# Kernel tuning notes

Hardware: AMD Instinct MI355X
Metric: run time of the kernel (lower is better)

The kernel has to match this reference:

```python
import jax, jax.numpy as jnp
import numpy as np

N_NODES = 100000
N_EDGES = 3200000
N_GRAPHS = 512
IN_DIM = 29   # NUM_COMPONENT_TYPES(15) + NUM_PARAMS(14)
HID = 128
LAT = 256


def setup_inputs() -> dict:
    key = jax.random.key(0)
    ks = jax.random.split(key, 16)
    x = jax.random.normal(ks[0], (N_NODES, IN_DIM), dtype=jnp.float32)
    edge_index = jax.random.randint(ks[1], (2, N_EDGES), 0, N_NODES, dtype=jnp.int64)
    batch = jnp.sort(jax.random.randint(ks[2], (N_NODES,), 0, N_GRAPHS, dtype=jnp.int64))

    def lin(k, fan_in, fan_out):
        kw, kb = jax.random.split(k)
        s = 1.0 / np.sqrt(fan_in)
        W = jax.random.uniform(kw, (fan_in, fan_out), minval=-s, maxval=s, dtype=jnp.float32)
        b = jax.random.uniform(kb, (fan_out,), minval=-s, maxval=s, dtype=jnp.float32)
        return W, b

    W1, b1 = lin(ks[3], IN_DIM, HID)
    W2, b2 = lin(ks[4], HID, HID)
    W3, b3 = lin(ks[5], HID, HID)
    Wmu, bmu = lin(ks[6], HID, LAT)
    Wlv, blv = lin(ks[7], HID, LAT)
    return {"x": x, "edge_index": edge_index, "batch": batch,
            "W1": W1, "b1": b1, "W2": W2, "b2": b2, "W3": W3, "b3": b3,
            "Wmu": Wmu, "bmu": bmu, "Wlv": Wlv, "blv": blv}


def _gcn_conv(h, W, b, src, dst, dis):
    # PyG GCNConv: out = D^-1/2 (A + I) D^-1/2 (h W) + b
    hw = h @ W                                   # [N, out]
    norm = dis[src] * dis[dst]                   # [E]
    agg = jax.ops.segment_sum(hw[src] * norm[:, None], dst, num_segments=h.shape[0])
    return agg + hw * (dis * dis)[:, None] + b   # self-loop term has norm dis[i]^2


def reference(x, edge_index, batch, W1, b1, W2, b2, W3, b3, Wmu, bmu, Wlv, blv):
    src, dst = edge_index[0], edge_index[1]
    # symmetric degree with self-loops (computed once, identical across layers)
    deg = jax.ops.segment_sum(jnp.ones(src.shape[0], jnp.float32), dst,
                              num_segments=x.shape[0]) + 1.0
    dis = jax.lax.rsqrt(deg)

    h = jax.nn.relu(_gcn_conv(x, W1, b1, src, dst, dis))
    h = jax.nn.relu(_gcn_conv(h, W2, b2, src, dst, dis))
    h = jax.nn.relu(_gcn_conv(h, W3, b3, src, dst, dis))

    # global_mean_pool over graph ids
    sums = jax.ops.segment_sum(h, batch, num_segments=N_GRAPHS)
    cnts = jax.ops.segment_sum(jnp.ones(h.shape[0], jnp.float32), batch,
                               num_segments=N_GRAPHS)
    pooled = sums / jnp.maximum(cnts, 1.0)[:, None]   # [G, HID]

    mu = pooled @ Wmu + bmu
    logvar = pooled @ Wlv + blv
    return (mu, logvar)
```

## Files before the change

### kernel.cpp

```cpp
#include <hip/hip_runtime.h>
#include <hip/hip_bf16.h>

#define N_NODES 100000
#define N_EDGES 3200000
#define N_GRAPHS 512
#define IN_DIM 29
#define HID 128
#define LAT 256
#define NB 391
#define CAP 9216

typedef unsigned int uint;
typedef unsigned short ushort;
typedef float v4f __attribute__((ext_vector_type(4)));
typedef short v8s __attribute__((ext_vector_type(8)));

__device__ __forceinline__ ushort f2bf(float f) {
    uint u = __float_as_uint(f);
    return (ushort)((u + 0x7FFFu + ((u >> 16) & 1u)) >> 16);
}
__device__ __forceinline__ float bf2f(ushort h) { return __uint_as_float(((uint)h) << 16); }
__device__ __forceinline__ float bf_lo(uint p) { return __uint_as_float(p << 16); }
__device__ __forceinline__ float bf_hi(uint p) { return __uint_as_float(p & 0xFFFF0000u); }
__device__ __forceinline__ uint pack2(float a, float b) {
    return (uint)f2bf(a) | ((uint)f2bf(b) << 16);
}

__device__ __forceinline__ void bfadd(float* a, uint4 q) {
    a[0] += bf_lo(q.x); a[1] += bf_hi(q.x);
    a[2] += bf_lo(q.y); a[3] += bf_hi(q.y);
    a[4] += bf_lo(q.z); a[5] += bf_hi(q.z);
    a[6] += bf_lo(q.w); a[7] += bf_hi(q.w);
}


__global__ __launch_bounds__(1024, 2) void k_binA(const int* __restrict__ src, const int* __restrict__ dst,
                                                  int* __restrict__ bktCnt, int* __restrict__ packed, int e) {
    __shared__ int hist[NB];
    __shared__ int base[NB];
    int t = threadIdx.x;
    for (int i = t; i < NB; i += 1024) hist[i] = 0;
    __syncthreads();
    int d[8], s[8];
    const int blockStart = blockIdx.x * 8192;
    #pragma unroll
    for (int k = 0; k < 8; ++k) {
        int idx = blockStart + k * 1024 + t;
        if (idx < e) {
            d[k] = dst[idx];
            s[k] = src[idx];
            atomicAdd(&hist[d[k] >> 8], 1);
        } else d[k] = -1;
    }
    __syncthreads();
    for (int i = t; i < NB; i += 1024) {
        int c = hist[i];
        base[i] = c ? atomicAdd(&bktCnt[i], c) : 0;
    }
    __syncthreads();
    #pragma unroll
    for (int k = 0; k < 8; ++k) {
        if (d[k] >= 0) {
            int b = d[k] >> 8;
            int pos = atomicAdd(&base[b], 1);
            if (pos < CAP) packed[b * CAP + pos] = ((d[k] & 255) << 17) | s[k];
        }
    }
}

__global__ __launch_bounds__(512) void k_bscan(const int* __restrict__ bktCnt, int* __restrict__ colStart) {
    __shared__ int sh[512];
    int t = threadIdx.x;
    int v = (t < NB) ? bktCnt[t] : 0;
    if (v > CAP) v = CAP;
    sh[t] = v;
    __syncthreads();
    for (int off = 1; off < 512; off <<= 1) {
        int x = (t >= off) ? sh[t - off] : 0;
        __syncthreads();
        sh[t] += x;
        __syncthreads();
    }
    int excl = sh[t] - v;
    if (t <= NB) colStart[t] = excl;
}

__global__ __launch_bounds__(1024, 2) void k_binB(const int* __restrict__ bktCnt, const int* __restrict__ colStart,
                                                  const int* __restrict__ packed, int* __restrict__ col,
                                                  int* __restrict__ rp, float* __restrict__ dis, int n) {
    __shared__ int cnt[8192];
    __shared__ int sh[1024];
    const int b = blockIdx.x;
    int cntB = bktCnt[b];
    if (cntB > CAP) cntB = CAP;
    const int segS = b * CAP;
    const int colBase = colStart[b];
    int t = threadIdx.x;
    #pragma unroll
    for (int k = 0; k < 8; ++k) cnt[t + k * 1024] = 0;
    __syncthreads();
    for (int j = t; j < cntB; j += 1024) {
        int pk = packed[segS + j];
        int key = ((pk >> 17) << 5) | ((pk & 0x1FFFF) >> 12);
        atomicAdd(&cnt[key], 1);
    }
    __syncthreads();
    int base8 = t << 3;
    int v[8];
    int sum = 0;
    #pragma unroll
    for (int k = 0; k < 8; ++k) { v[k] = cnt[base8 + k]; sum += v[k]; }
    sh[t] = sum;
    __syncthreads();
    for (int off = 1; off < 1024; off <<= 1) {
        int x = (t >= off) ? sh[t - off] : 0;
        __syncthreads();
        sh[t] += x;
        __syncthreads();
    }
    int run = colBase + sh[t] - sum;
    #pragma unroll
    for (int k = 0; k < 8; ++k) { cnt[base8 + k] = run; run += v[k]; }
    __syncthreads();
    if (t < 256) {
        int node = (b << 8) + t;
        int start = cnt[t << 5];
        int next = (t == 255) ? (colBase + cntB) : cnt[(t + 1) << 5];
        int deg = next - start;
        if (node <= n) rp[node] = start;
        if (node < n) dis[node] = rsqrtf((float)deg + 1.0f);
    }
    __syncthreads();
    for (int j = t; j < cntB; j += 1024) {
        int pk = packed[segS + j];
        int key = ((pk >> 17) << 5) | ((pk & 0x1FFFF) >> 12);
        int pos = atomicAdd(&cnt[key], 1);
        col[pos] = pk & 0x1FFFF;
    }
}


__device__ __forceinline__ void pack_one(const float* W, ushort* hi, ushort* lo, int Ksrc, int idx) {
    int j = idx & 7;
    int lane = (idx >> 3) & 63;
    int nt = (idx >> 9) & 7;
    int ks = idx >> 12;
    int k = ks * 32 + (lane >> 4) * 8 + j;
    int n = nt * 16 + (lane & 15);
    float v = (k < Ksrc) ? W[k * 128 + n] : 0.f;
    ushort h = f2bf(v);
    ushort l = f2bf(v - bf2f(h));
    hi[idx] = h;
    lo[idx] = l;
}

__global__ __launch_bounds__(256) void k_pack_all(const float* __restrict__ W1, const float* __restrict__ W2,
                                                  const float* __restrict__ W3,
                                                  ushort* w1h, ushort* w1l, ushort* w2h, ushort* w2l,
                                                  ushort* w3h, ushort* w3l, int* __restrict__ bktCnt) {
    int idx = blockIdx.x * 256 + threadIdx.x;
    if (idx < NB) bktCnt[idx] = 0;
    if (idx < 4096) {
        pack_one(W1, w1h, w1l, IN_DIM, idx);
    } else if (idx < 4096 + 16384) {
        pack_one(W2, w2h, w2l, HID, idx - 4096);
    } else if (idx < 4096 + 32768) {
        pack_one(W3, w3h, w3l, HID, idx - 4096 - 16384);
    }
}


__global__ __launch_bounds__(256) void k_scale(const float* __restrict__ x, const float* __restrict__ dis,
                                               float* __restrict__ xt, int n) {
    int idx = blockIdx.x * 256 + threadIdx.x;
    if (idx >= n * 32) return;
    int row = idx >> 5, k = idx & 31;
    float v = (k < IN_DIM) ? x[(size_t)row * IN_DIM + k] * dis[row] : 0.f;
    xt[idx] = v;
}

__global__ __launch_bounds__(256, 6) void k_agg29(const float* __restrict__ xt, const int* __restrict__ rp,
                                                  const int* __restrict__ col, const float* __restrict__ dis,
                                                  float* __restrict__ y, int n) {
    int node = (int)((blockIdx.x * 256 + threadIdx.x) >> 3);
    if (node >= n) return;
    int c4 = (threadIdx.x & 7) << 2;
    int s = rp[node], e = rp[node + 1];
    v4f A = (v4f){0.f, 0.f, 0.f, 0.f};
    v4f B = (v4f){0.f, 0.f, 0.f, 0.f};
    int j = s;
    for (; j + 7 < e; j += 8) {
        int c0 = col[j],     c1 = col[j + 1], c2 = col[j + 2], c3 = col[j + 3];
        int c4i = col[j + 4], c5 = col[j + 5], c6 = col[j + 6], c7 = col[j + 7];
        v4f q0 = *(const v4f*)(xt + ((size_t)c0 << 5) + c4);
        v4f q1 = *(const v4f*)(xt + ((size_t)c1 << 5) + c4);
        v4f q2 = *(const v4f*)(xt + ((size_t)c2 << 5) + c4);
        v4f q3 = *(const v4f*)(xt + ((size_t)c3 << 5) + c4);
        v4f q4 = *(const v4f*)(xt + ((size_t)c4i << 5) + c4);
        v4f q5 = *(const v4f*)(xt + ((size_t)c5 << 5) + c4);
        v4f q6 = *(const v4f*)(xt + ((size_t)c6 << 5) + c4);
        v4f q7 = *(const v4f*)(xt + ((size_t)c7 << 5) + c4);
        A += q0; B += q1; A += q2; B += q3;
        A += q4; B += q5; A += q6; B += q7;
    }
    if (j + 3 < e) {
        int c0 = col[j], c1 = col[j + 1], c2 = col[j + 2], c3 = col[j + 3];
        v4f q0 = *(const v4f*)(xt + ((size_t)c0 << 5) + c4);
        v4f q1 = *(const v4f*)(xt + ((size_t)c1 << 5) + c4);
        v4f q2 = *(const v4f*)(xt + ((size_t)c2 << 5) + c4);
        v4f q3 = *(const v4f*)(xt + ((size_t)c3 << 5) + c4);
        A += q0; B += q1; A += q2; B += q3;
        j += 4;
    }
    for (; j < e; ++j) {
        int c = col[j];
        A += *(const v4f*)(xt + ((size_t)c << 5) + c4);
    }
    A += *(const v4f*)(xt + ((size_t)node << 5) + c4);
    float dv = dis[node];
    v4f o = (A + B) * dv;
    *(v4f*)(y + ((size_t)node << 5) + c4) = o;
}

__global__ __launch_bounds__(256, 6) void k_gemm1(const float* __restrict__ in,
                                                  const ushort* __restrict__ Whi,
                                                  const ushort* __restrict__ Wlo,
                                                  const float* __restrict__ bias,
                                                  ushort* __restrict__ out, int n) {
    const int wave = threadIdx.x >> 6;
    const int lane = threadIdx.x & 63;
    const int m0 = (blockIdx.x * 4 + wave) * 16;
    if (m0 >= n) return;
    int row = m0 + (lane & 15);
    if (row >= n) row = n - 1;
    const int kh = (lane >> 4) * 8;
    const float* rptr = in + ((size_t)row << 5) + kh;

    v4f acc[8];
    #pragma unroll
    for (int t = 0; t < 8; ++t) acc[t] = (v4f){0.f, 0.f, 0.f, 0.f};

    float a[8];
    #pragma unroll
    for (int j = 0; j < 8; ++j) a[j] = rptr[j];
    v8s ahi, alo;
    #pragma unroll
    for (int j = 0; j < 8; ++j) {
        ushort h = f2bf(a[j]);
        ushort l = f2bf(a[j] - bf2f(h));
        ahi[j] = (short)h;
        alo[j] = (short)l;
    }
    const ushort* bh = Whi + (size_t)lane * 8;
    const ushort* bl = Wlo + (size_t)lane * 8;
    #pragma unroll
    for (int nt = 0; nt < 8; ++nt) {
        v8s bhi = *(const v8s*)(bh + nt * 512);
        v8s blo = *(const v8s*)(bl + nt * 512);
        acc[nt] = __builtin_amdgcn_mfma_f32_16x16x32_bf16(ahi, bhi, acc[nt], 0, 0, 0);
        acc[nt] = __builtin_amdgcn_mfma_f32_16x16x32_bf16(ahi, blo, acc[nt], 0, 0, 0);
        acc[nt] = __builtin_amdgcn_mfma_f32_16x16x32_bf16(alo, bhi, acc[nt], 0, 0, 0);
    }

    const int orow0 = m0 + (lane >> 4) * 4;
    const int col0 = lane & 15;
    float bb[8];
    #pragma unroll
    for (int nt = 0; nt < 8; ++nt) bb[nt] = bias[nt * 16 + col0];
    #pragma unroll
    for (int r = 0; r < 4; ++r) {
        int orow = orow0 + r;
        if (orow < n) {
            #pragma unroll
            for (int nt = 0; nt < 8; ++nt)
                out[(size_t)orow * 128 + nt * 16 + col0] = f2bf(fmaxf(acc[nt][r] + bb[nt], 0.f));
        }
    }
}


__global__ __launch_bounds__(256, 6) void k_gemm_mfma_bf(const ushort* __restrict__ in,
                                                         const ushort* __restrict__ Whi,
                                                         const ushort* __restrict__ Wlo,
                                                         const float* __restrict__ dis,
                                                         ushort* __restrict__ out, int n) {
    const int wave = threadIdx.x >> 6;
    const int lane = threadIdx.x & 63;
    const int m0 = (blockIdx.x * 4 + wave) * 16;
    if (m0 >= n) return;
    int row = m0 + (lane & 15);
    if (row >= n) row = n - 1;
    const int kh = (lane >> 4) * 8;
    const ushort* rptr = in + (size_t)row * 128 + kh;

    v4f acc[8];
    #pragma unroll
    for (int t = 0; t < 8; ++t) acc[t] = (v4f){0.f, 0.f, 0.f, 0.f};

    #pragma unroll
    for (int ks = 0; ks < 4; ++ks) {
        v8s a = *(const v8s*)(rptr + ks * 32);
        const ushort* bh = Whi + (size_t)(ks * 8) * 512 + (size_t)lane * 8;
        const ushort* bl = Wlo + (size_t)(ks * 8) * 512 + (size_t)lane * 8;
        #pragma unroll
        for (int nt = 0; nt < 8; ++nt) {
            v8s bhi = *(const v8s*)(bh + nt * 512);
            v8s blo = *(const v8s*)(bl + nt * 512);
            acc[nt] = __builtin_amdgcn_mfma_f32_16x16x32_bf16(a, bhi, acc[nt], 0, 0, 0);
            acc[nt] = __builtin_amdgcn_mfma_f32_16x16x32_bf16(a, blo, acc[nt], 0, 0, 0);
        }
    }

    const int orow0 = m0 + (lane >> 4) * 4;
    const int col0 = lane & 15;
    #pragma unroll
    for (int r = 0; r < 4; ++r) {
        int orow = orow0 + r;
        if (orow < n) {
            float dv = dis[orow];
            #pragma unroll
            for (int nt = 0; nt < 8; ++nt)
                out[(size_t)orow * 128 + nt * 16 + col0] = f2bf(acc[nt][r] * dv);
        }
    }
}


__global__ __launch_bounds__(256, 6) void k_agg(const ushort* __restrict__ hws, const int* __restrict__ rp,
                                                const int* __restrict__ col, const float* __restrict__ dis,
                                                const float* __restrict__ bias, ushort* __restrict__ out, int n) {
    int g = blockIdx.x * 32 + (threadIdx.x >> 3);
    int node = (g < n) ? g : g - n;
    if (g >= 2 * n) return;
    int c8 = ((g < n) ? 0 : 64) + ((threadIdx.x & 7) << 3);
    int s = rp[node], e = rp[node + 1];
    float A[8] = {0.f, 0.f, 0.f, 0.f, 0.f, 0.f, 0.f, 0.f};
    float B[8] = {0.f, 0.f, 0.f, 0.f, 0.f, 0.f, 0.f, 0.f};
    int j = s;
    for (; j + 7 < e; j += 8) {
        int c0 = col[j],     c1 = col[j + 1], c2 = col[j + 2], c3 = col[j + 3];
        int c4 = col[j + 4], c5 = col[j + 5], c6 = col[j + 6], c7 = col[j + 7];
        uint4 q0 = *(const uint4*)(hws + ((size_t)c0 << 7) + c8);
        uint4 q1 = *(const uint4*)(hws + ((size_t)c1 << 7) + c8);
        uint4 q2 = *(const uint4*)(hws + ((size_t)c2 << 7) + c8);
        uint4 q3 = *(const uint4*)(hws + ((size_t)c3 << 7) + c8);
        uint4 q4 = *(const uint4*)(hws + ((size_t)c4 << 7) + c8);
        uint4 q5 = *(const uint4*)(hws + ((size_t)c5 << 7) + c8);
        uint4 q6 = *(const uint4*)(hws + ((size_t)c6 << 7) + c8);
        uint4 q7 = *(const uint4*)(hws + ((size_t)c7 << 7) + c8);
        bfadd(A, q0); bfadd(B, q1); bfadd(A, q2); bfadd(B, q3);
        bfadd(A, q4); bfadd(B, q5); bfadd(A, q6); bfadd(B, q7);
    }
    if (j + 3 < e) {
        int c0 = col[j], c1 = col[j + 1], c2 = col[j + 2], c3 = col[j + 3];
        uint4 q0 = *(const uint4*)(hws + ((size_t)c0 << 7) + c8);
        uint4 q1 = *(const uint4*)(hws + ((size_t)c1 << 7) + c8);
        uint4 q2 = *(const uint4*)(hws + ((size_t)c2 << 7) + c8);
        uint4 q3 = *(const uint4*)(hws + ((size_t)c3 << 7) + c8);
        bfadd(A, q0); bfadd(B, q1); bfadd(A, q2); bfadd(B, q3);
        j += 4;
    }
    for (; j < e; ++j) {
        int c = col[j];
        uint4 q = *(const uint4*)(hws + ((size_t)c << 7) + c8);
        bfadd(A, q);
    }
    uint4 qs = *(const uint4*)(hws + ((size_t)node << 7) + c8);
    bfadd(A, qs);
    float dv = dis[node];
    float4 bv0 = *(const float4*)(bias + c8);
    float4 bv1 = *(const float4*)(bias + c8 + 4);
    float r0 = fmaxf(dv * (A[0] + B[0]) + bv0.x, 0.f);
    float r1 = fmaxf(dv * (A[1] + B[1]) + bv0.y, 0.f);
    float r2 = fmaxf(dv * (A[2] + B[2]) + bv0.z, 0.f);
    float r3 = fmaxf(dv * (A[3] + B[3]) + bv0.w, 0.f);
    float r4 = fmaxf(dv * (A[4] + B[4]) + bv1.x, 0.f);
    float r5 = fmaxf(dv * (A[5] + B[5]) + bv1.y, 0.f);
    float r6 = fmaxf(dv * (A[6] + B[6]) + bv1.z, 0.f);
    float r7 = fmaxf(dv * (A[7] + B[7]) + bv1.w, 0.f);
    uint4 o;
    o.x = pack2(r0, r1);
    o.y = pack2(r2, r3);
    o.z = pack2(r4, r5);
    o.w = pack2(r6, r7);
    *(uint4*)(out + (size_t)node * 128 + c8) = o;
}


__global__ __launch_bounds__(256) void k_pool_head(const ushort* __restrict__ h, const int* __restrict__ batch,
                                                   const float* __restrict__ Wmu, const float* __restrict__ bmu,
                                                   const float* __restrict__ Wlv, const float* __restrict__ blv,
                                                   float* __restrict__ out, int n) {
    int g = blockIdx.x;
    int t = threadIdx.x;
    int lo = 0, hi = n;
    while (lo < hi) { int m = (lo + hi) >> 1; if (batch[m] < g) lo = m + 1; else hi = m; }
    int start = lo;
    hi = n;
    while (lo < hi) { int m = (lo + hi) >> 1; if (batch[m] < g + 1) lo = m + 1; else hi = m; }
    int end = lo;

    __shared__ float sh0[256];
    __shared__ float sh1[256];
    __shared__ float pooled[128];
    int lane = t & 63;
    int grp = t >> 6;
    float a0 = 0.f, a1 = 0.f;
    for (int i = start + grp; i < end; i += 4) {
        uint q = *(const uint*)(h + (size_t)i * 128 + lane * 2);
        a0 += bf_lo(q);
        a1 += bf_hi(q);
    }
    sh0[t] = a0;
    sh1[t] = a1;
    __syncthreads();
    if (t < 64) {
        float cnt = (float)(end - start);
        float inv = 1.0f / fmaxf(cnt, 1.0f);
        float s0 = sh0[t] + sh0[t + 64] + sh0[t + 128] + sh0[t + 192];
        float s1 = sh1[t] + sh1[t + 64] + sh1[t + 128] + sh1[t + 192];
        pooled[t * 2] = s0 * inv;
        pooled[t * 2 + 1] = s1 * inv;
    }
    __syncthreads();
    float amu = bmu[t], alv = blv[t];
    for (int k = 0; k < 128; k += 4) {
        float p0 = pooled[k], p1 = pooled[k + 1], p2 = pooled[k + 2], p3 = pooled[k + 3];
        amu += p0 * Wmu[(k + 0) * 256 + t] + p1 * Wmu[(k + 1) * 256 + t]
             + p2 * Wmu[(k + 2) * 256 + t] + p3 * Wmu[(k + 3) * 256 + t];
        alv += p0 * Wlv[(k + 0) * 256 + t] + p1 * Wlv[(k + 1) * 256 + t]
             + p2 * Wlv[(k + 2) * 256 + t] + p3 * Wlv[(k + 3) * 256 + t];
    }
    out[(size_t)g * 256 + t] = amu;
    out[(size_t)N_GRAPHS * 256 + (size_t)g * 256 + t] = alv;
}


extern "C" void kernel_launch(void* const* d_in, const int* in_sizes, int n_in,
                              void* d_out, int out_size, void* d_ws, size_t ws_size,
                              hipStream_t stream) {
    const float* x    = (const float*)d_in[0];
    const int*   eidx = (const int*)d_in[1];
    const int*   batch= (const int*)d_in[2];
    const float* W1   = (const float*)d_in[3];
    const float* b1   = (const float*)d_in[4];
    const float* W2   = (const float*)d_in[5];
    const float* b2   = (const float*)d_in[6];
    const float* W3   = (const float*)d_in[7];
    const float* b3   = (const float*)d_in[8];
    const float* Wmu  = (const float*)d_in[9];
    const float* bmu  = (const float*)d_in[10];
    const float* Wlv  = (const float*)d_in[11];
    const float* blv  = (const float*)d_in[12];
    float* out = (float*)d_out;

    const int N = N_NODES, E = N_EDGES;
    const int* srcp = eidx;
    const int* dstp = eidx + E;

    ushort* w1h = (ushort*)d_ws;
    ushort* w1l = w1h + 4096;
    ushort* w2h = w1l + 4096;
    ushort* w2l = w2h + 16384;
    ushort* w3h = w2l + 16384;
    ushort* w3l = w3h + 16384;
    ushort* A   = w3l + 16384;
    ushort* B   = A + (size_t)N * 128;
    float*  dis = (float*)(B + (size_t)N * 128);
    int*   rp   = (int*)(dis + N);
    int*   bktCnt   = rp + (N + 2);
    int*   colStart = bktCnt + 512;
    int*   packed = colStart + 512;
    int*   col    = packed + (size_t)NB * CAP;

    float* xt = (float*)A;
    float* yv = xt + (size_t)N * 32;

    const int gE8192 = (E + 8191) / 8192;

    k_pack_all<<<144, 256, 0, stream>>>(W1, W2, W3, w1h, w1l, w2h, w2l, w3h, w3l, bktCnt);

    k_binA<<<gE8192, 1024, 0, stream>>>(srcp, dstp, bktCnt, packed, E);
    k_bscan<<<1, 512, 0, stream>>>(bktCnt, colStart);
    k_binB<<<NB, 1024, 0, stream>>>(bktCnt, colStart, packed, col, rp, dis, N);

    const int gGemm = (N + 63) / 64;
    const int gAgg  = (2 * N + 31) / 32;

    k_scale<<<(N * 32 + 255) / 256, 256, 0, stream>>>(x, dis, xt, N);
    k_agg29<<<(N * 8 + 255) / 256, 256, 0, stream>>>(xt, rp, col, dis, yv, N);
    k_gemm1<<<gGemm, 256, 0, stream>>>(yv, w1h, w1l, b1, B, N);

    k_gemm_mfma_bf<<<gGemm, 256, 0, stream>>>(B, w2h, w2l, dis, A, N);
    k_agg<<<gAgg, 256, 0, stream>>>(A, rp, col, dis, b2, B, N);
    k_gemm_mfma_bf<<<gGemm, 256, 0, stream>>>(B, w3h, w3l, dis, A, N);
    k_agg<<<gAgg, 256, 0, stream>>>(A, rp, col, dis, b3, B, N);
    k_pool_head<<<N_GRAPHS, 256, 0, stream>>>(B, batch, Wmu, bmu, Wlv, blv, out, N);
}
```

Before: 482.8 us.

## Fuse input scaling into binning, widen GEMM tiles, split aggregation by halves

Three separate changes. The x*dis scaling now happens inside k_binB, which removes the k_scale launch. The hidden-layer GEMM computes 32 rows per wave instead of 16, so each weight fragment load is reused twice, and the occupancy hint drops from 6 to 4. The aggregation kernel is split into two launches, one per 64-column half, replacing the interleaved single launch, so each pass gathers over a narrower slice of the features and may get better cache locality. The cost is an extra launch per layer and higher register pressure in the GEMM.

```diff
diff --git a/kernel.cpp b/kernel.cpp
--- a/kernel.cpp
+++ b/kernel.cpp
@@ -87,9 +87,11 @@
 
 __global__ __launch_bounds__(1024, 2) void k_binB(const int* __restrict__ bktCnt, const int* __restrict__ colStart,
                                                   const int* __restrict__ packed, int* __restrict__ col,
-                                                  int* __restrict__ rp, float* __restrict__ dis, int n) {
+                                                  int* __restrict__ rp, float* __restrict__ dis,
+                                                  const float* __restrict__ x, float* __restrict__ xt, int n) {
     __shared__ int cnt[8192];
     __shared__ int sh[1024];
+    __shared__ float sdis[256];
     const int b = blockIdx.x;
     int cntB = bktCnt[b];
     if (cntB > CAP) cntB = CAP;
@@ -113,9 +115,9 @@
     sh[t] = sum;
     __syncthreads();
     for (int off = 1; off < 1024; off <<= 1) {
-        int x = (t >= off) ? sh[t - off] : 0;
+        int x2 = (t >= off) ? sh[t - off] : 0;
         __syncthreads();
-        sh[t] += x;
+        sh[t] += x2;
         __syncthreads();
     }
     int run = colBase + sh[t] - sum;
@@ -127,10 +129,21 @@
         int start = cnt[t << 5];
         int next = (t == 255) ? (colBase + cntB) : cnt[(t + 1) << 5];
         int deg = next - start;
+        float dv = rsqrtf((float)deg + 1.0f);
+        sdis[t] = dv;
         if (node <= n) rp[node] = start;
-        if (node < n) dis[node] = rsqrtf((float)deg + 1.0f);
-    }
-    __syncthreads();
+        if (node < n) dis[node] = dv;
+    }
+    __syncthreads();
+    for (int idx = t; idx < 256 * 32; idx += 1024) {
+        int loc = idx >> 5;
+        int node = (b << 8) + loc;
+        if (node < n) {
+            int k = idx & 31;
+            float vv = (k < IN_DIM) ? x[(size_t)node * IN_DIM + k] * sdis[loc] : 0.f;
+            xt[((size_t)node << 5) + k] = vv;
+        }
+    }
     for (int j = t; j < cntB; j += 1024) {
         int pk = packed[segS + j];
         int key = ((pk >> 17) << 5) | ((pk & 0x1FFFF) >> 12);
@@ -169,15 +182,6 @@
     }
 }
 
-
-__global__ __launch_bounds__(256) void k_scale(const float* __restrict__ x, const float* __restrict__ dis,
-                                               float* __restrict__ xt, int n) {
-    int idx = blockIdx.x * 256 + threadIdx.x;
-    if (idx >= n * 32) return;
-    int row = idx >> 5, k = idx & 31;
-    float v = (k < IN_DIM) ? x[(size_t)row * IN_DIM + k] * dis[row] : 0.f;
-    xt[idx] = v;
-}
 
 __global__ __launch_bounds__(256, 6) void k_agg29(const float* __restrict__ xt, const int* __restrict__ rp,
                                                   const int* __restrict__ col, const float* __restrict__ dis,
@@ -279,40 +283,49 @@
 }
 
 
-__global__ __launch_bounds__(256, 6) void k_gemm_mfma_bf(const ushort* __restrict__ in,
-                                                         const ushort* __restrict__ Whi,
-                                                         const ushort* __restrict__ Wlo,
-                                                         const float* __restrict__ dis,
-                                                         ushort* __restrict__ out, int n) {
+__global__ __launch_bounds__(256, 4) void k_gemm_bf32(const ushort* __restrict__ in,
+                                                      const ushort* __restrict__ Whi,
+                                                      const ushort* __restrict__ Wlo,
+                                                      const float* __restrict__ dis,
+                                                      ushort* __restrict__ out, int n) {
     const int wave = threadIdx.x >> 6;
     const int lane = threadIdx.x & 63;
-    const int m0 = (blockIdx.x * 4 + wave) * 16;
+    const int m0 = (blockIdx.x * 4 + wave) * 32;
     if (m0 >= n) return;
-    int row = m0 + (lane & 15);
-    if (row >= n) row = n - 1;
+    int row0 = m0 + (lane & 15);
+    int row1 = row0 + 16;
+    if (row0 >= n) row0 = n - 1;
+    if (row1 >= n) row1 = n - 1;
     const int kh = (lane >> 4) * 8;
-    const ushort* rptr = in + (size_t)row * 128 + kh;
-
-    v4f acc[8];
-    #pragma unroll
-    for (int t = 0; t < 8; ++t) acc[t] = (v4f){0.f, 0.f, 0.f, 0.f};
+    const ushort* rp0 = in + (size_t)row0 * 128 + kh;
+    const ushort* rp1 = in + (size_t)row1 * 128 + kh;
+
+    v4f acc0[8], acc1[8];
+    #pragma unroll
+    for (int t = 0; t < 8; ++t) {
+        acc0[t] = (v4f){0.f, 0.f, 0.f, 0.f};
+        acc1[t] = (v4f){0.f, 0.f, 0.f, 0.f};
+    }
 
     #pragma unroll
     for (int ks = 0; ks < 4; ++ks) {
-        v8s a = *(const v8s*)(rptr + ks * 32);
+        v8s a0 = *(const v8s*)(rp0 + ks * 32);
+        v8s a1 = *(const v8s*)(rp1 + ks * 32);
         const ushort* bh = Whi + (size_t)(ks * 8) * 512 + (size_t)lane * 8;
         const ushort* bl = Wlo + (size_t)(ks * 8) * 512 + (size_t)lane * 8;
         #pragma unroll
         for (int nt = 0; nt < 8; ++nt) {
             v8s bhi = *(const v8s*)(bh + nt * 512);
             v8s blo = *(const v8s*)(bl + nt * 512);
-            acc[nt] = __builtin_amdgcn_mfma_f32_16x16x32_bf16(a, bhi, acc[nt], 0, 0, 0);
-            acc[nt] = __builtin_amdgcn_mfma_f32_16x16x32_bf16(a, blo, acc[nt], 0, 0, 0);
+            acc0[nt] = __builtin_amdgcn_mfma_f32_16x16x32_bf16(a0, bhi, acc0[nt], 0, 0, 0);
+            acc0[nt] = __builtin_amdgcn_mfma_f32_16x16x32_bf16(a0, blo, acc0[nt], 0, 0, 0);
+            acc1[nt] = __builtin_amdgcn_mfma_f32_16x16x32_bf16(a1, bhi, acc1[nt], 0, 0, 0);
+            acc1[nt] = __builtin_amdgcn_mfma_f32_16x16x32_bf16(a1, blo, acc1[nt], 0, 0, 0);
         }
     }
 
+    const int col0 = lane & 15;
     const int orow0 = m0 + (lane >> 4) * 4;
-    const int col0 = lane & 15;
     #pragma unroll
     for (int r = 0; r < 4; ++r) {
         int orow = orow0 + r;
@@ -320,7 +333,14 @@
             float dv = dis[orow];
             #pragma unroll
             for (int nt = 0; nt < 8; ++nt)
-                out[(size_t)orow * 128 + nt * 16 + col0] = f2bf(acc[nt][r] * dv);
+                out[(size_t)orow * 128 + nt * 16 + col0] = f2bf(acc0[nt][r] * dv);
+        }
+        int orow2 = orow + 16;
+        if (orow2 < n) {
+            float dv = dis[orow2];
+            #pragma unroll
+            for (int nt = 0; nt < 8; ++nt)
+                out[(size_t)orow2 * 128 + nt * 16 + col0] = f2bf(acc1[nt][r] * dv);
         }
     }
 }
@@ -328,11 +348,11 @@
 
 __global__ __launch_bounds__(256, 6) void k_agg(const ushort* __restrict__ hws, const int* __restrict__ rp,
                                                 const int* __restrict__ col, const float* __restrict__ dis,
-                                                const float* __restrict__ bias, ushort* __restrict__ out, int n) {
-    int g = blockIdx.x * 32 + (threadIdx.x >> 3);
-    int node = (g < n) ? g : g - n;
-    if (g >= 2 * n) return;
-    int c8 = ((g < n) ? 0 : 64) + ((threadIdx.x & 7) << 3);
+                                                const float* __restrict__ bias, ushort* __restrict__ out,
+                                                int n, int half) {
+    int node = (int)(blockIdx.x * 32 + (threadIdx.x >> 3));
+    if (node >= n) return;
+    int c8 = half * 64 + ((threadIdx.x & 7) << 3);
     int s = rp[node], e = rp[node + 1];
     float A[8] = {0.f, 0.f, 0.f, 0.f, 0.f, 0.f, 0.f, 0.f};
     float B[8] = {0.f, 0.f, 0.f, 0.f, 0.f, 0.f, 0.f, 0.f};
@@ -482,18 +502,20 @@
 
     k_binA<<<gE8192, 1024, 0, stream>>>(srcp, dstp, bktCnt, packed, E);
     k_bscan<<<1, 512, 0, stream>>>(bktCnt, colStart);
-    k_binB<<<NB, 1024, 0, stream>>>(bktCnt, colStart, packed, col, rp, dis, N);
-
-    const int gGemm = (N + 63) / 64;
-    const int gAgg  = (2 * N + 31) / 32;
-
-    k_scale<<<(N * 32 + 255) / 256, 256, 0, stream>>>(x, dis, xt, N);
-    k_agg29<<<(N * 8 + 255) / 256, 256, 0, stream>>>(xt, rp, col, dis, yv, N);
-    k_gemm1<<<gGemm, 256, 0, stream>>>(yv, w1h, w1l, b1, B, N);
-
-    k_gemm_mfma_bf<<<gGemm, 256, 0, stream>>>(B, w2h, w2l, dis, A, N);
-    k_agg<<<gAgg, 256, 0, stream>>>(A, rp, col, dis, b2, B, N);
-    k_gemm_mfma_bf<<<gGemm, 256, 0, stream>>>(B, w3h, w3l, dis, A, N);
-    k_agg<<<gAgg, 256, 0, stream>>>(A, rp, col, dis, b3, B, N);
+    k_binB<<<NB, 1024, 0, stream>>>(bktCnt, colStart, packed, col, rp, dis, x, xt, N);
+
+    const int gGemm1 = (N + 63) / 64;
+    const int gGemm2 = (N + 127) / 128;
+    const int gAggH  = (N * 8 + 255) / 256;
+
+    k_agg29<<<gAggH, 256, 0, stream>>>(xt, rp, col, dis, yv, N);
+    k_gemm1<<<gGemm1, 256, 0, stream>>>(yv, w1h, w1l, b1, B, N);
+
+    k_gemm_bf32<<<gGemm2, 256, 0, stream>>>(B, w2h, w2l, dis, A, N);
+    k_agg<<<gAggH, 256, 0, stream>>>(A, rp, col, dis, b2, B, N, 0);
+    k_agg<<<gAggH, 256, 0, stream>>>(A, rp, col, dis, b2, B, N, 1);
+    k_gemm_bf32<<<gGemm2, 256, 0, stream>>>(B, w3h, w3l, dis, A, N);
+    k_agg<<<gAggH, 256, 0, stream>>>(A, rp, col, dis, b3, B, N, 0);
+    k_agg<<<gAggH, 256, 0, stream>>>(A, rp, col, dis, b3, B, N, 1);
     k_pool_head<<<N_GRAPHS, 256, 0, stream>>>(B, batch, Wmu, bmu, Wlv, blv, out, N);
 }
```

Result: no change. 487.3 us (+0.9%).
